# Performance work log

Measured on AMD Instinct MI355X. Metric: run time of the kernel, lower is better.

Reference implementation:

```python
import jax, jax.numpy as jnp
import numpy as np

ALPHA = 0.5
NUM_CLASSES = 86
FEAT = 256
N = 131072


def setup_inputs() -> dict:
    key = jax.random.key(0)
    k1, k2, k3 = jax.random.split(key, 3)
    features = jax.random.normal(k1, (N, FEAT), dtype=jnp.float32)
    labels = jax.random.randint(k2, (N,), 0, NUM_CLASSES)
    # non-trainable centers buffer, RandomNormal init (stddev 0.05 like keras default)
    centers = 0.05 * jax.random.normal(k3, (NUM_CLASSES, FEAT), dtype=jnp.float32)
    return {"features": features, "labels": labels, "centers": centers}


def reference(features, labels, centers):
    labels = labels.reshape(-1)
    # gather per-sample centers: [N, F]
    centers_batch = centers[labels]
    d = features - centers_batch
    # tf.nn.l2_loss = 0.5 * sum(x^2)
    loss = 0.5 * jnp.sum(d * d)
    # appear_times via unique_with_counts == per-class occurrence count gathered back
    counts = jax.ops.segment_sum(
        jnp.ones((labels.shape[0],), dtype=jnp.float32), labels,
        num_segments=NUM_CLASSES)  # [C]
    appear_times = counts[labels][:, None]  # [N, 1]
    diff = ALPHA * (-d) / (1.0 + appear_times)  # (centers_batch - features) scaled
    # tf.scatter_sub accumulates duplicate indices
    new_centers = centers.at[labels].add(-diff)
    return loss, new_centers
```

## Files before the change

### kernel.cpp

```cpp
#include <hip/hip_runtime.h>

#define ALPHA 0.5f
#define NCLS 86
#define FEAT 256
#define NTOT 131072

constexpr int K   = 32;
constexpr int BLK = 256;
constexpr int CH  = NTOT / K;
constexpr int WCH = CH / 4;

constexpr size_t WS_S    = 0;
constexpr size_t WS_CNT  = (size_t)K * NCLS * FEAT;
constexpr size_t WS_L2   = WS_CNT + (size_t)K * NCLS;
constexpr size_t WS_CLS  = WS_L2 + (size_t)K * NCLS;

__global__ __launch_bounds__(BLK) void ctc_main(
    const float4* __restrict__ feat4, const int* __restrict__ labels,
    float* __restrict__ S_part, float* __restrict__ cnt_part,
    float* __restrict__ l2_part)
{
    const int k = blockIdx.x % K;
    const int c = blockIdx.x / K;
    const int wave = threadIdx.x >> 6;
    const int lane = threadIdx.x & 63;

    const int wbase = k * CH + wave * WCH;

    float4 acc = {0.f, 0.f, 0.f, 0.f};
    float  acc2 = 0.f;
    int    cnt  = 0;

    for (int it = 0; it < WCH; it += 64) {
        const int lab = labels[wbase + it + lane];
        unsigned long long m = __ballot(lab == c);
        cnt += __popcll(m);
        while (m) {
            const int b = (int)__ffsll((long long)m) - 1;
            m &= m - 1;
            const float4 v = feat4[(size_t)(wbase + it + b) * 64 + lane];
            acc.x += v.x; acc.y += v.y; acc.z += v.z; acc.w += v.w;
            acc2  += v.x * v.x + v.y * v.y + v.z * v.z + v.w * v.w;
        }
    }

    for (int off = 32; off; off >>= 1)
        acc2 += __shfl_down(acc2, off, 64);

    __shared__ float4 ls4[4][64];
    __shared__ float  lcnt[4], ll2[4];
    ls4[wave][lane] = acc;
    if (lane == 0) { lcnt[wave] = (float)cnt; ll2[wave] = acc2; }
    __syncthreads();

    const int t = threadIdx.x;
    const float* lf = (const float*)ls4;
    const float s = lf[t] + lf[FEAT + t] + lf[2 * FEAT + t] + lf[3 * FEAT + t];
    S_part[((size_t)k * NCLS + c) * FEAT + t] = s;
    if (t == 0) {
        cnt_part[k * NCLS + c] = lcnt[0] + lcnt[1] + lcnt[2] + lcnt[3];
        l2_part[k * NCLS + c]  = ll2[0] + ll2[1] + ll2[2] + ll2[3];
    }
}

__global__ __launch_bounds__(256) void ctc_finalize(
    const float* __restrict__ centers, const float* __restrict__ S_part,
    const float* __restrict__ cnt_part, const float* __restrict__ l2_part,
    float* __restrict__ class_loss, float* __restrict__ out_centers)
{
    const int c = blockIdx.x;
    const int t = threadIdx.x;

    float S = 0.f;
    for (int k = 0; k < K; ++k)
        S += S_part[((size_t)k * NCLS + c) * FEAT + t];

    __shared__ float sn, sl2;
    if (t == 0) {
        float a = 0.f, b = 0.f;
        for (int k = 0; k < K; ++k) {
            a += cnt_part[k * NCLS + c];
            b += l2_part[k * NCLS + c];
        }
        sn = a; sl2 = b;
    }
    __syncthreads();

    const float n  = sn;
    const float cc = centers[c * FEAT + t];
    out_centers[c * FEAT + t] = cc + ALPHA * (S - n * cc) / (1.f + n);

    float part = 0.5f * n * cc * cc - S * cc;
    for (int off = 32; off; off >>= 1) part += __shfl_down(part, off, 64);

    __shared__ float red[4];
    const int wv = t >> 6, ln = t & 63;
    if (ln == 0) red[wv] = part;
    __syncthreads();
    if (t == 0)
        class_loss[c] = red[0] + red[1] + red[2] + red[3] + 0.5f * sl2;
}

__global__ void ctc_loss_write(const float* __restrict__ class_loss,
                               float* __restrict__ out)
{
    const int l = threadIdx.x;
    float v = (l < NCLS) ? class_loss[l] : 0.f;
    if (l + 64 < NCLS) v += class_loss[l + 64];
    for (int off = 32; off; off >>= 1) v += __shfl_down(v, off, 64);
    if (l == 0) out[0] = v;
}

extern "C" void kernel_launch(void* const* d_in, const int* in_sizes, int n_in,
                              void* d_out, int out_size, void* d_ws, size_t ws_size,
                              hipStream_t stream)
{
    const float* feat    = (const float*)d_in[0];
    const int*   labels  = (const int*)d_in[1];
    const float* centers = (const float*)d_in[2];
    float* out = (float*)d_out;
    float* ws  = (float*)d_ws;

    float* S_part     = ws + WS_S;
    float* cnt_part   = ws + WS_CNT;
    float* l2_part    = ws + WS_L2;
    float* class_loss = ws + WS_CLS;

    ctc_main<<<NCLS * K, BLK, 0, stream>>>(
        (const float4*)feat, labels, S_part, cnt_part, l2_part);

    ctc_finalize<<<NCLS, 256, 0, stream>>>(
        centers, S_part, cnt_part, l2_part, class_loss, out + 1);

    ctc_loss_write<<<1, 64, 0, stream>>>(class_loss, out);
}
```

Before: 38.31 us.

## Use single-wave blocks with int4 label loads and class-major partial layout

The main kernel now uses 64-thread single-wave blocks over twice as many sample chunks, so the LDS cross-wave reduction and __syncthreads go away. Each lane loads four labels at once as an int4 and runs four ballots, which cuts the label-load instruction count. Partial sums are stored class-major so the finalize kernel reads them contiguously. In exchange the finalize kernel reduces twice as many partials, and each tiny block holds fewer waves for latency hiding.

```diff
diff --git a/kernel.cpp b/kernel.cpp
--- a/kernel.cpp
+++ b/kernel.cpp
@@ -5,61 +5,56 @@
 #define FEAT 256
 #define NTOT 131072
 
-constexpr int K   = 32;
-constexpr int BLK = 256;
+constexpr int K   = 64;
 constexpr int CH  = NTOT / K;
-constexpr int WCH = CH / 4;
+constexpr int ITS = CH / 4 / 64;
 
-constexpr size_t WS_S    = 0;
-constexpr size_t WS_CNT  = (size_t)K * NCLS * FEAT;
-constexpr size_t WS_L2   = WS_CNT + (size_t)K * NCLS;
-constexpr size_t WS_CLS  = WS_L2 + (size_t)K * NCLS;
+constexpr size_t WS_S   = 0;
+constexpr size_t WS_CNT = (size_t)NCLS * K * FEAT;
+constexpr size_t WS_L2  = WS_CNT + (size_t)NCLS * K;
+constexpr size_t WS_CLS = WS_L2 + (size_t)NCLS * K;
 
-__global__ __launch_bounds__(BLK) void ctc_main(
-    const float4* __restrict__ feat4, const int* __restrict__ labels,
-    float* __restrict__ S_part, float* __restrict__ cnt_part,
+__global__ __launch_bounds__(64) void ctc_main(
+    const float4* __restrict__ feat4, const int4* __restrict__ lab4,
+    float4* __restrict__ S_part4, float* __restrict__ cnt_part,
     float* __restrict__ l2_part)
 {
     const int k = blockIdx.x % K;
     const int c = blockIdx.x / K;
-    const int wave = threadIdx.x >> 6;
-    const int lane = threadIdx.x & 63;
-
-    const int wbase = k * CH + wave * WCH;
+    const int lane = threadIdx.x;
+    const int base = k * CH;
 
     float4 acc = {0.f, 0.f, 0.f, 0.f};
     float  acc2 = 0.f;
     int    cnt  = 0;
 
-    for (int it = 0; it < WCH; it += 64) {
-        const int lab = labels[wbase + it + lane];
-        unsigned long long m = __ballot(lab == c);
-        cnt += __popcll(m);
-        while (m) {
-            const int b = (int)__ffsll((long long)m) - 1;
-            m &= m - 1;
-            const float4 v = feat4[(size_t)(wbase + it + b) * 64 + lane];
-            acc.x += v.x; acc.y += v.y; acc.z += v.z; acc.w += v.w;
-            acc2  += v.x * v.x + v.y * v.y + v.z * v.z + v.w * v.w;
+    for (int it = 0; it < ITS * 64; it += 64) {
+        const int4 L = lab4[base / 4 + it + lane];
+        unsigned long long m0 = __ballot(L.x == c);
+        unsigned long long m1 = __ballot(L.y == c);
+        unsigned long long m2 = __ballot(L.z == c);
+        unsigned long long m3 = __ballot(L.w == c);
+        cnt += __popcll(m0) + __popcll(m1) + __popcll(m2) + __popcll(m3);
+#define DRAIN(mm, j)                                                        \
+        while (mm) {                                                       \
+            const int b = (int)__ffsll((long long)mm) - 1;                 \
+            mm &= mm - 1;                                                  \
+            const float4 v = feat4[(size_t)(base + (it + b) * 4 + j) * 64  \
+                                   + lane];                                \
+            acc.x += v.x; acc.y += v.y; acc.z += v.z; acc.w += v.w;        \
+            acc2  += v.x * v.x + v.y * v.y + v.z * v.z + v.w * v.w;        \
         }
+        DRAIN(m0, 0) DRAIN(m1, 1) DRAIN(m2, 2) DRAIN(m3, 3)
+#undef DRAIN
     }
+
+    S_part4[((size_t)c * K + k) * 64 + lane] = acc;
 
     for (int off = 32; off; off >>= 1)
         acc2 += __shfl_down(acc2, off, 64);
-
-    __shared__ float4 ls4[4][64];
-    __shared__ float  lcnt[4], ll2[4];
-    ls4[wave][lane] = acc;
-    if (lane == 0) { lcnt[wave] = (float)cnt; ll2[wave] = acc2; }
-    __syncthreads();
-
-    const int t = threadIdx.x;
-    const float* lf = (const float*)ls4;
-    const float s = lf[t] + lf[FEAT + t] + lf[2 * FEAT + t] + lf[3 * FEAT + t];
-    S_part[((size_t)k * NCLS + c) * FEAT + t] = s;
-    if (t == 0) {
-        cnt_part[k * NCLS + c] = lcnt[0] + lcnt[1] + lcnt[2] + lcnt[3];
-        l2_part[k * NCLS + c]  = ll2[0] + ll2[1] + ll2[2] + ll2[3];
+    if (lane == 0) {
+        cnt_part[c * K + k] = (float)cnt;
+        l2_part[c * K + k]  = acc2;
     }
 }
 
@@ -73,14 +68,14 @@
 
     float S = 0.f;
     for (int k = 0; k < K; ++k)
-        S += S_part[((size_t)k * NCLS + c) * FEAT + t];
+        S += S_part[((size_t)c * K + k) * FEAT + t];
 
     __shared__ float sn, sl2;
     if (t == 0) {
         float a = 0.f, b = 0.f;
         for (int k = 0; k < K; ++k) {
-            a += cnt_part[k * NCLS + c];
-            b += l2_part[k * NCLS + c];
+            a += cnt_part[c * K + k];
+            b += l2_part[c * K + k];
         }
         sn = a; sl2 = b;
     }
@@ -126,8 +121,9 @@
     float* l2_part    = ws + WS_L2;
     float* class_loss = ws + WS_CLS;
 
-    ctc_main<<<NCLS * K, BLK, 0, stream>>>(
-        (const float4*)feat, labels, S_part, cnt_part, l2_part);
+    ctc_main<<<NCLS * K, 64, 0, stream>>>(
+        (const float4*)feat, (const int4*)labels,
+        (float4*)S_part, cnt_part, l2_part);
 
     ctc_finalize<<<NCLS, 256, 0, stream>>>(
         centers, S_part, cnt_part, l2_part, class_loss, out + 1);
```

New measurement: 35.81 us. -6.5%, faster.
